# Performance work log

Hardware: AMD Instinct MI355X
Metric: run time of the kernel (lower is better)

The kernel has to match this reference:

```python
import jax, jax.numpy as jnp
import numpy as np
import math

PERIODS = [4, 2, 1]          # period_num[-3:] sorted desc
SEQ, PRED, CH = 192, 96, 8
TOPM, DM = 20, 512
N_TRAIN, BSZ = 10000, 32


def decompose_mg(data):
    # data: [N, L, C] -> mg: [P, N, L, C], offset-removed (last step per period)
    N, L, C = data.shape
    mgs = []
    for g in PERIODS:
        cur = data.reshape(N, L // g, g, C).mean(axis=2)   # pooled
        cur = jnp.repeat(cur, g, axis=1)                   # repeat_interleave
        mgs.append(cur)
    mg = jnp.stack(mgs, axis=0)                            # [P, N, L, C]
    offset = mg[:, :, -1:, :]
    return mg - offset


def l2norm(x, eps=1e-12):
    n = jnp.sqrt(jnp.sum(x * x, axis=-1, keepdims=True))
    return x / jnp.maximum(n, eps)


def setup_inputs() -> dict:
    key = jax.random.key(0)
    ks = jax.random.split(key, 10)
    F = SEQ * CH
    return {
        "x": jax.random.normal(ks[0], (BSZ, SEQ, CH), dtype=jnp.float32),
        "index": jax.random.randint(ks[1], (BSZ,), 0, N_TRAIN),
        "train_data_all": jax.random.normal(ks[2], (N_TRAIN, SEQ, CH), dtype=jnp.float32),
        "y_data_all": jax.random.normal(ks[3], (N_TRAIN, PRED, CH), dtype=jnp.float32),
        "W_sim": jax.random.normal(ks[4], (F, F), dtype=jnp.float32) / math.sqrt(F),
        "b_sim": jax.random.normal(ks[5], (F,), dtype=jnp.float32) * 0.01,
        "Wq": jax.random.normal(ks[6], (CH, DM), dtype=jnp.float32) / math.sqrt(CH),
        "bq": jax.random.normal(ks[7], (DM,), dtype=jnp.float32) * 0.01,
        "Wk": jax.random.normal(ks[8], (CH, DM), dtype=jnp.float32) / math.sqrt(CH),
        "bk": jax.random.normal(ks[9], (DM,), dtype=jnp.float32) * 0.01,
    }


def reference(x, index, train_data_all, y_data_all, W_sim, b_sim, Wq, bq, Wk, bk):
    P = len(PERIODS)
    bsz = x.shape[0]
    n_train = train_data_all.shape[0]

    # multi-period decomposition (prepare_dataset + retrieve)
    train_mg = decompose_mg(train_data_all)   # [P, N, SEQ, CH]
    y_mg = decompose_mg(y_data_all)           # [P, N, PRED, CH]
    x_mg = decompose_mg(x)                    # [P, B, SEQ, CH]

    # periodic_batch_corr: shared linear then cosine similarity
    bx = x_mg.reshape(P, bsz, -1) @ W_sim + b_sim           # [P, B, F]
    ax = train_mg.reshape(P, n_train, -1) @ W_sim + b_sim   # [P, N, F]
    sim = jnp.einsum('pbf,pnf->pbn', l2norm(bx), l2norm(ax))

    # self-exclusion sliding mask (train=True)
    win = 2 * (SEQ + PRED) - 1
    slid = jnp.arange(win)[None, :] + (index - SEQ - PRED + 1)[:, None]
    slid = jnp.clip(slid, 0, n_train - 1)
    mask = jnp.zeros((bsz, n_train), dtype=bool).at[
        jnp.arange(bsz)[:, None], slid].set(True)
    sim = jnp.where(mask[None], -jnp.inf, sim)

    # top-m retrieval
    _, topm_idx = jax.lax.top_k(sim, TOPM)                  # [P, B, TOPM]

    # gather neighbors per period
    gather = jax.vmap(lambda src, i: src[i])                # over period axis
    k = gather(train_mg, topm_idx)                          # [P, B, M, SEQ, CH]
    v = gather(y_mg, topm_idx)                              # [P, B, M, PRED, CH]

    # cross attention (shared projections across periods)
    q_emb = x_mg @ Wq + bq                                  # [P, B, S, D]
    k_emb = k @ Wk + bk                                     # [P, B, M, T, D]
    scores = jnp.einsum('pbsd,pbmtd->pbsmt', q_emb, k_emb) / math.sqrt(DM)
    S = scores.shape[2]
    w = jax.nn.softmax(scores.reshape(P, bsz, S, TOPM * S), axis=-1)
    w = w.reshape(P, bsz, S, TOPM, S)
    nw = w.sum(axis=-1).sum(axis=2)                         # [P, B, M]
    nw = jax.nn.softmax(nw, axis=-1)
    out = jnp.einsum('pbm,pbmlc->pblc', nw, v)              # [P, B, PRED, CH]
    return out
```

## Files before the change

### kernel.cpp

```cpp
#include <hip/hip_runtime.h>
#include <hip/hip_bf16.h>
#include <math.h>

#define NPER 3
#define SEQL 192
#define PREDL 96
#define CH 8
#define FD 1536
#define NT 10000
#define BS 32
#define PB 96
#define TOPM 20
#define DM 512
#define HALFW 287
#define NROWS 30000
#define NRP2 10112
#define NRB2 79
#define NCB 12
#define PCOLS 24
#define NWG2 (NRB2*NCB)
#define NJ 3840
#define K0R 384
#define K1R 768
#define K2R 1536
#define KS 16
#define KSD 8
#define NCH 4
#define CHSZ (NT/NCH)
#define NWTG 4080
#define NB_DOT (NRB2*KSD)
#define RSQRT_DM 0.04419417382415922f

typedef __attribute__((ext_vector_type(8))) short bf16x8;
typedef __attribute__((ext_vector_type(4))) float f32x4;
typedef __attribute__((address_space(3))) short lds_short_t;
typedef __attribute__((address_space(1))) const short glb_short_t;

__device__ inline float bflo(unsigned u){ return __uint_as_float(u << 16); }
__device__ inline float bfhi(unsigned u){ return __uint_as_float(u & 0xFFFF0000u); }
__device__ inline float bf2f(unsigned short u){ return __uint_as_float((unsigned)u << 16); }
__device__ inline unsigned short f2bf(float v){
  __hip_bfloat16 h = __float2bfloat16(v);
  return *reinterpret_cast<unsigned short*>(&h);
}

template<int L>
__device__ __forceinline__ void dec_body(const float* __restrict__ data,
                                         float* __restrict__ mg,
                                         __hip_bfloat16* __restrict__ m0,
                                         __hip_bfloat16* __restrict__ m1,
                                         __hip_bfloat16* __restrict__ m2,
                                         __hip_bfloat16* __restrict__ trH,
                                         __hip_bfloat16* __restrict__ trL,
                                         int N, int n, float* fpool) {
  float* row = fpool;
  float* m4  = fpool + L*CH;
  float* m2s = fpool + L*CH + (L/4)*CH;
  const float* src = data + (size_t)n*L*CH;
  for (int e = threadIdx.x; e < L*CH/4; e += 256)
    *reinterpret_cast<float4*>(&row[e*4]) = *reinterpret_cast<const float4*>(&src[e*4]);
  __syncthreads();
  for (int i = threadIdx.x; i < (L/4)*CH; i += 256) {
    int j = i >> 3, c = i & 7;
    m4[i] = (row[(4*j)*CH+c] + row[(4*j+1)*CH+c] + row[(4*j+2)*CH+c] + row[(4*j+3)*CH+c]) * 0.25f;
  }
  for (int i = threadIdx.x; i < (L/2)*CH; i += 256) {
    int j = i >> 3, c = i & 7;
    m2s[i] = (row[(2*j)*CH+c] + row[(2*j+1)*CH+c]) * 0.5f;
  }
  __syncthreads();
  if (mg) {
    size_t plane = (size_t)N*L*CH;
    size_t base  = (size_t)n*L*CH;
    for (int e = threadIdx.x; e < L*CH/4; e += 256) {
      int i = e*4;
      int l = i >> 3, c0 = i & 7;
      float v0[4], v1[4], v2[4];
      #pragma unroll
      for (int j=0;j<4;j++) {
        int c = c0 + j;
        v0[j] = m4[(l>>2)*CH+c] - m4[(L/4-1)*CH+c];
        v1[j] = m2s[(l>>1)*CH+c] - m2s[(L/2-1)*CH+c];
        v2[j] = row[i+j] - row[(L-1)*CH+c];
      }
      *reinterpret_cast<float4*>(&mg[base+i])           = make_float4(v0[0],v0[1],v0[2],v0[3]);
      *reinterpret_cast<float4*>(&mg[plane+base+i])     = make_float4(v1[0],v1[1],v1[2],v1[3]);
      *reinterpret_cast<float4*>(&mg[2*plane+base+i])   = make_float4(v2[0],v2[1],v2[2],v2[3]);
    }
  }
  if (m0) {
    unsigned short* p0 = (unsigned short*)m0 + (size_t)n*K0R;
    unsigned short* p1 = (unsigned short*)m1 + (size_t)n*K1R;
    unsigned short* p2 = (unsigned short*)m2 + (size_t)n*K2R;
    for (int e = threadIdx.x; e < K0R/4; e += 256) {
      int i = e*4, c0 = i & 7;
      ushort4 u;
      u.x = f2bf(m4[i]   - m4[(L/4-1)*CH + c0]);
      u.y = f2bf(m4[i+1] - m4[(L/4-1)*CH + c0+1]);
      u.z = f2bf(m4[i+2] - m4[(L/4-1)*CH + c0+2]);
      u.w = f2bf(m4[i+3] - m4[(L/4-1)*CH + c0+3]);
      *reinterpret_cast<ushort4*>(&p0[i]) = u;
    }
    for (int e = threadIdx.x; e < K1R/4; e += 256) {
      int i = e*4, c0 = i & 7;
      ushort4 u;
      u.x = f2bf(m2s[i]   - m2s[(L/2-1)*CH + c0]);
      u.y = f2bf(m2s[i+1] - m2s[(L/2-1)*CH + c0+1]);
      u.z = f2bf(m2s[i+2] - m2s[(L/2-1)*CH + c0+2]);
      u.w = f2bf(m2s[i+3] - m2s[(L/2-1)*CH + c0+3]);
      *reinterpret_cast<ushort4*>(&p1[i]) = u;
    }
    for (int e = threadIdx.x; e < K2R/4; e += 256) {
      int i = e*4, c0 = i & 7;
      ushort4 u;
      u.x = f2bf(row[i]   - row[(L-1)*CH + c0]);
      u.y = f2bf(row[i+1] - row[(L-1)*CH + c0+1]);
      u.z = f2bf(row[i+2] - row[(L-1)*CH + c0+2]);
      u.w = f2bf(row[i+3] - row[(L-1)*CH + c0+3]);
      *reinterpret_cast<ushort4*>(&p2[i]) = u;
    }
  }
  if (trH) {
    unsigned short* h = (unsigned short*)trH + (size_t)n*L*CH;
    unsigned short* l = (unsigned short*)trL + (size_t)n*L*CH;
    for (int e = threadIdx.x; e < L*CH/4; e += 256) {
      int i = e*4;
      ushort4 uh, ul;
      uh.x = f2bf(row[i]);   ul.x = f2bf(row[i]   - bf2f(uh.x));
      uh.y = f2bf(row[i+1]); ul.y = f2bf(row[i+1] - bf2f(uh.y));
      uh.z = f2bf(row[i+2]); ul.z = f2bf(row[i+2] - bf2f(uh.z));
      uh.w = f2bf(row[i+3]); ul.w = f2bf(row[i+3] - bf2f(uh.w));
      *reinterpret_cast<ushort4*>(&h[i]) = uh;
      *reinterpret_cast<ushort4*>(&l[i]) = ul;
    }
  }
}

__device__ __forceinline__ void wtg_body(const float* __restrict__ W,
                                         __hip_bfloat16* __restrict__ wt0,
                                         __hip_bfloat16* __restrict__ wt1,
                                         __hip_bfloat16* __restrict__ wt2,
                                         const float* __restrict__ Wq,
                                         const float* __restrict__ bq,
                                         const float* __restrict__ Wk,
                                         const float* __restrict__ bk,
                                         float* __restrict__ cst,
                                         int wb, float* fpool) {
  int bxx = wb / 48, byy = wb % 48;
  if (bxx == 84) {
    if (byy != 0) return;
    int tt = threadIdx.x;
    if (tt < 64) {
      int c = tt >> 3, e = tt & 7;
      float s = 0.f;
      for (int d=0; d<DM; d++) s += Wq[c*DM+d] * Wk[e*DM+d];
      cst[tt] = s;
    } else if (tt < 72) {
      int c = tt - 64; float s=0.f;
      for (int d=0;d<DM;d++) s += Wq[c*DM+d]*bk[d];
      cst[tt] = s;
    } else if (tt < 80) {
      int e = tt - 72; float s=0.f;
      for (int d=0;d<DM;d++) s += Wk[e*DM+d]*bq[d];
      cst[tt] = s;
    } else if (tt == 80) {
      float s=0.f;
      for (int d=0;d<DM;d++) s += bq[d]*bk[d];
      cst[80] = s;
    }
    return;
  }
  int G, kr0, Kred;
  __hip_bfloat16* Wt;
  if (bxx < 12)      { G = 4; kr0 = bxx*32;      Kred = K0R; Wt = wt0; }
  else if (bxx < 36) { G = 2; kr0 = (bxx-12)*32; Kred = K1R; Wt = wt1; }
  else               { G = 1; kr0 = (bxx-36)*32; Kred = K2R; Wt = wt2; }
  int f0 = byy*32;
  int k0 = kr0*G;
  int tid = threadIdx.x, tx = tid & 31, ty = tid >> 5;
  for (int i = ty; i < 32*G; i += 8)
    fpool[i*33 + tx] = W[(size_t)(k0+i)*FD + f0 + tx];
  __syncthreads();
  for (int fl = ty; fl < 32; fl += 8) {
    float s = 0.f;
    for (int i=0;i<G;i++) s += fpool[(((tx>>3)*G+i)*8 + (tx&7))*33 + fl];
    Wt[(size_t)(f0+fl)*Kred + kr0 + tx] = __float2bfloat16(s);
  }
}

__global__ __launch_bounds__(256) void k_front(const float* __restrict__ x,
                                               const float* __restrict__ train,
                                               float* __restrict__ x_mg,
                                               __hip_bfloat16* __restrict__ m0,
                                               __hip_bfloat16* __restrict__ m1,
                                               __hip_bfloat16* __restrict__ m2,
                                               __hip_bfloat16* __restrict__ trH,
                                               __hip_bfloat16* __restrict__ trL,
                                               const float* __restrict__ W,
                                               __hip_bfloat16* __restrict__ wt0,
                                               __hip_bfloat16* __restrict__ wt1,
                                               __hip_bfloat16* __restrict__ wt2,
                                               const float* __restrict__ Wq,
                                               const float* __restrict__ bq,
                                               const float* __restrict__ Wk,
                                               const float* __restrict__ bk,
                                               float* __restrict__ cst) {
  __shared__ float fpool[128*33];
  int bid = blockIdx.x;
  if (bid < NT) {
    dec_body<SEQL>(train, nullptr, m0, m1, m2, trH, trL, NT, bid, fpool);
  } else if (bid < NT + NWTG) {
    wtg_body(W, wt0, wt1, wt2, Wq, bq, Wk, bk, cst, bid - NT, fpool);
  } else {
    dec_body<SEQL>(x, x_mg, nullptr, nullptr, nullptr, nullptr, nullptr,
                   BS, bid - NT - NWTG, fpool);
  }
}

__global__ __launch_bounds__(256) void k_bx_part(const float* __restrict__ xmg,
                                                 const float* __restrict__ W,
                                                 float* __restrict__ bxp) {
  __shared__ float xs[PB][17];
  __shared__ float Ws[16][65];
  int f0 = blockIdx.x * 64;
  int ks = blockIdx.y;
  int kbase = ks * (FD/KS);
  int tid = threadIdx.x;
  int fl = tid & 63, gp = tid >> 6;
  float acc[24];
  #pragma unroll
  for (int j=0;j<24;j++) acc[j]=0.f;
  for (int k0 = kbase; k0 < kbase + FD/KS; k0 += 16) {
    for (int e = tid; e < PB*16; e += 256) {
      int r = e >> 4, k = e & 15;
      xs[r][k] = xmg[(size_t)r*FD + k0 + k];
    }
    for (int e = tid; e < 16*64; e += 256) {
      int k = e >> 6, f = e & 63;
      Ws[k][f] = W[(size_t)(k0+k)*FD + f0 + f];
    }
    __syncthreads();
    #pragma unroll
    for (int kk = 0; kk < 16; kk++) {
      float w = Ws[kk][fl];
      #pragma unroll
      for (int j=0;j<24;j++) acc[j] += w * xs[gp + 4*j][kk];
    }
    __syncthreads();
  }
  #pragma unroll
  for (int j=0;j<24;j++) {
    int pb = gp + 4*j;
    bxp[((size_t)ks*PB + pb)*FD + f0 + fl] = acc[j];
  }
}

__global__ __launch_bounds__(256) void k_bxnorm(const float* __restrict__ bxp,
                                                const float* __restrict__ bsim,
                                                float* __restrict__ u_out,
                                                float* __restrict__ cpb) {
  __shared__ float rowv[FD];
  __shared__ float r1[256], r2[256];
  __shared__ float invs;
  int pb = blockIdx.x, tid = threadIdx.x;
  float s2 = 0.f, sb = 0.f;
  for (int f = tid; f < FD; f += 256) {
    float s = 0.f;
    #pragma unroll
    for (int ks=0; ks<KS; ks++) s += bxp[((size_t)ks*PB + pb)*FD + f];
    s += bsim[f];
    rowv[f] = s;
    s2 += s*s; sb += s*bsim[f];
  }
  r1[tid]=s2; r2[tid]=sb; __syncthreads();
  for (int off=128; off>0; off>>=1) {
    if (tid<off) { r1[tid]+=r1[tid+off]; r2[tid]+=r2[tid+off]; }
    __syncthreads();
  }
  if (tid==0) {
    float iv = 1.f / fmaxf(sqrtf(r1[0]), 1e-12f);
    invs = iv;
    cpb[pb] = r2[0] * iv;
  }
  __syncthreads();
  float iv = invs;
  for (int f = tid; f < FD; f += 256) u_out[(size_t)pb*FD + f] = rowv[f]*iv;
}

__global__ __launch_bounds__(256) void k_t_part(const float* __restrict__ u,
                                                const float* __restrict__ W,
                                                float* __restrict__ tp) {
  __shared__ float us[PB][17];
  __shared__ float Wt[64][17];
  int k0 = blockIdx.x * 64;
  int ks = blockIdx.y;
  int fbase = ks * (FD/KS);
  int tid = threadIdx.x;
  int kl = tid & 63, gp = tid >> 6;
  float acc[24];
  #pragma unroll
  for (int j=0;j<24;j++) acc[j]=0.f;
  for (int fc = fbase; fc < fbase + FD/KS; fc += 16) {
    for (int e = tid; e < PB*16; e += 256) {
      int r = e >> 4, f = e & 15;
      us[r][f] = u[(size_t)r*FD + fc + f];
    }
    for (int e = tid; e < 64*16; e += 256) {
      int k = e >> 4, f = e & 15;
      Wt[k][f] = W[(size_t)(k0+k)*FD + fc + f];
    }
    __syncthreads();
    #pragma unroll
    for (int ff = 0; ff < 16; ff++) {
      float w = Wt[kl][ff];
      #pragma unroll
      for (int j=0;j<24;j++) acc[j] += w * us[gp + 4*j][ff];
    }
    __syncthreads();
  }
  #pragma unroll
  for (int j=0;j<24;j++) {
    int pb = gp + 4*j;
    tp[((size_t)ks*PB + pb)*FD + k0 + kl] = acc[j];
  }
}

__global__ __launch_bounds__(192) void k_tred_adj(const float* __restrict__ tp,
                                                  __hip_bfloat16* __restrict__ tadjH,
                                                  __hip_bfloat16* __restrict__ tadjL) {
  __shared__ float ts[SEQL*CH];
  __shared__ float Tc[CH];
  int pb = blockIdx.x;
  int p = pb / BS;
  int g = (p==0) ? 4 : (p==1) ? 2 : 1;
  int l = threadIdx.x;
  #pragma unroll
  for (int c=0;c<CH;c++) {
    float s = 0.f;
    #pragma unroll
    for (int ks=0; ks<KS; ks++) s += tp[((size_t)ks*PB + pb)*FD + l*CH + c];
    ts[l*CH+c] = s;
  }
  __syncthreads();
  if (l < CH) {
    float s=0.f;
    for (int j=0;j<SEQL;j++) s += ts[j*CH+l];
    Tc[l] = s;
  }
  __syncthreads();
  int j0 = (l/g)*g;
  bool last = (j0 == SEQL-g);
  float ig = 1.f/(float)g;
  unsigned short* th = (unsigned short*)tadjH;
  unsigned short* tl = (unsigned short*)tadjL;
  #pragma unroll
  for (int c=0;c<CH;c++) {
    float s = 0.f;
    for (int jj=0;jj<g;jj++) s += ts[(j0+jj)*CH+c];
    float v = s*ig - (last ? Tc[c]*ig : 0.f);
    unsigned short hv = f2bf(v);
    th[(size_t)pb*FD + l*CH+c] = hv;
    tl[(size_t)pb*FD + l*CH+c] = f2bf(v - bf2f(hv));
  }
}

__device__ __forceinline__ void norm_body(const short* __restrict__ A,
                                          const short* __restrict__ B,
                                          int K, int p, int seg,
                                          const float* __restrict__ bsim,
                                          float* __restrict__ part,
                                          short* pool) {
  short* lA = pool;
  short* lB = pool + 128*32;
  int q = NWG2 >> 3, r = NWG2 & 7;
  int xcd = seg & 7, pos = seg >> 3;
  int wgid = (xcd < r ? xcd*(q+1) : r*(q+1) + (xcd-r)*q) + pos;
  int rb = wgid / NCB, cb = wgid - rb*NCB;
  int row0 = rb*128, col0 = cb*128;
  int tid = threadIdx.x, lane = tid & 63, wid = tid >> 6;
  int wr = (wid>>1)*64, wc = (wid&1)*64;

  size_t aoff[2], boff[2];
  int ldsb[2];
  #pragma unroll
  for (int i=0;i<2;i++) {
    int lrow = (wid*2+i)*16 + (lane>>2);
    int sl = lane & 3;
    int ss = (sl - lrow - (lrow>>2)) & 3;
    aoff[i] = (size_t)(row0 + lrow)*K + 8*ss;
    boff[i] = (size_t)(col0 + lrow)*K + 8*ss;
    ldsb[i] = (wid*2+i)*16*32;
  }

  f32x4 acc[4][4];
  #pragma unroll
  for (int m=0;m<4;m++)
    #pragma unroll
    for (int n=0;n<4;n++) acc[m][n] = (f32x4){0.f,0.f,0.f,0.f};

  int kslot = lane >> 4;
  for (int k0 = 0; k0 < K; k0 += 32) {
    #pragma unroll
    for (int i=0;i<2;i++) {
      __builtin_amdgcn_global_load_lds((glb_short_t*)(A + aoff[i] + k0),
                                       (lds_short_t*)&lA[ldsb[i]], 16, 0, 0);
      __builtin_amdgcn_global_load_lds((glb_short_t*)(B + boff[i] + k0),
                                       (lds_short_t*)&lB[ldsb[i]], 16, 0, 0);
    }
    __syncthreads();
    bf16x8 af[4], bfr[4];
    #pragma unroll
    for (int m=0;m<4;m++) {
      int rr = wr + m*16 + (lane&15);
      int s = (kslot + rr + (rr>>2)) & 3;
      af[m] = *(const bf16x8*)&lA[rr*32 + s*8];
    }
    #pragma unroll
    for (int n=0;n<4;n++) {
      int rr = wc + n*16 + (lane&15);
      int s = (kslot + rr + (rr>>2)) & 3;
      bfr[n] = *(const bf16x8*)&lB[rr*32 + s*8];
    }
    #pragma unroll
    for (int m=0;m<4;m++)
      #pragma unroll
      for (int n=0;n<4;n++)
        acc[m][n] = __builtin_amdgcn_mfma_f32_16x16x32_bf16(af[m], bfr[n], acc[m][n], 0, 0, 0);
    __syncthreads();
  }

  float bv[4];
  #pragma unroll
  for (int n=0;n<4;n++) bv[n] = bsim[col0 + wc + n*16 + (lane&15)];
  int pslot = cb*2 + (wid&1);
  #pragma unroll
  for (int m=0;m<4;m++) {
    #pragma unroll
    for (int j=0;j<4;j++) {
      float s = 0.f;
      #pragma unroll
      for (int n=0;n<4;n++) { float v = acc[m][n][j] + bv[n]; s += v*v; }
      s += __shfl_xor(s, 1); s += __shfl_xor(s, 2);
      s += __shfl_xor(s, 4); s += __shfl_xor(s, 8);
      if ((lane & 15) == 0) {
        int rr = row0 + wr + m*16 + (lane>>4)*4 + j;
        part[((size_t)p*NRP2 + rr)*PCOLS + pslot] = s;
      }
    }
  }
}

__device__ __forceinline__ void dot_body(const short* __restrict__ AH,
                                         const short* __restrict__ AL,
                                         const short* __restrict__ BH,
                                         const short* __restrict__ BL,
                                         float* __restrict__ dotp,
                                         int dbid, short* pool) {
  short* lAH = pool;
  short* lAL = pool + 128*32;
  short* lBH = pool + 2*128*32;
  short* lBL = pool + 3*128*32;
  int ks = dbid & 7, cbn = dbid >> 3;
  int col0 = cbn * 128;
  int kbase = ks * (FD/KSD);
  int tid = threadIdx.x, lane = tid & 63, wid = tid >> 6;
  int wr = (wid>>1)*64, wc = (wid&1)*64;

  size_t aoff[2], boff[2];
  int ldsb[2];
  #pragma unroll
  for (int i=0;i<2;i++) {
    int lrow = (wid*2+i)*16 + (lane>>2);
    int sl = lane & 3;
    int ss = (sl - lrow - (lrow>>2)) & 3;
    aoff[i] = (size_t)lrow*FD + 8*ss;
    boff[i] = (size_t)(col0 + lrow)*FD + 8*ss;
    ldsb[i] = (wid*2+i)*16*32;
  }

  f32x4 acc[4][4];
  #pragma unroll
  for (int m=0;m<4;m++)
    #pragma unroll
    for (int n=0;n<4;n++) acc[m][n] = (f32x4){0.f,0.f,0.f,0.f};

  int kslot = lane >> 4;
  for (int k0 = kbase; k0 < kbase + FD/KSD; k0 += 32) {
    #pragma unroll
    for (int i=0;i<2;i++) {
      __builtin_amdgcn_global_load_lds((glb_short_t*)(AH + aoff[i] + k0),
                                       (lds_short_t*)&lAH[ldsb[i]], 16, 0, 0);
      __builtin_amdgcn_global_load_lds((glb_short_t*)(AL + aoff[i] + k0),
                                       (lds_short_t*)&lAL[ldsb[i]], 16, 0, 0);
      __builtin_amdgcn_global_load_lds((glb_short_t*)(BH + boff[i] + k0),
                                       (lds_short_t*)&lBH[ldsb[i]], 16, 0, 0);
      __builtin_amdgcn_global_load_lds((glb_short_t*)(BL + boff[i] + k0),
                                       (lds_short_t*)&lBL[ldsb[i]], 16, 0, 0);
    }
    __syncthreads();
    bf16x8 ah[4], al[4], bh[4], bl[4];
    #pragma unroll
    for (int m=0;m<4;m++) {
      int rr = wr + m*16 + (lane&15);
      int s = (kslot + rr + (rr>>2)) & 3;
      ah[m] = *(const bf16x8*)&lAH[rr*32 + s*8];
      al[m] = *(const bf16x8*)&lAL[rr*32 + s*8];
    }
    #pragma unroll
    for (int n=0;n<4;n++) {
      int rr = wc + n*16 + (lane&15);
      int s = (kslot + rr + (rr>>2)) & 3;
      bh[n] = *(const bf16x8*)&lBH[rr*32 + s*8];
      bl[n] = *(const bf16x8*)&lBL[rr*32 + s*8];
    }
    #pragma unroll
    for (int m=0;m<4;m++)
      #pragma unroll
      for (int n=0;n<4;n++) {
        acc[m][n] = __builtin_amdgcn_mfma_f32_16x16x32_bf16(ah[m], bh[n], acc[m][n], 0, 0, 0);
        acc[m][n] = __builtin_amdgcn_mfma_f32_16x16x32_bf16(ah[m], bl[n], acc[m][n], 0, 0, 0);
        acc[m][n] = __builtin_amdgcn_mfma_f32_16x16x32_bf16(al[m], bh[n], acc[m][n], 0, 0, 0);
      }
    __syncthreads();
  }

  #pragma unroll
  for (int m=0;m<4;m++) {
    int prow = wr + m*16 + (lane>>4)*4;
    if (prow >= PB) continue;
    #pragma unroll
    for (int n=0;n<4;n++) {
      int ncol = col0 + wc + n*16 + (lane&15);
      if (ncol >= NT) continue;
      #pragma unroll
      for (int j=0;j<4;j++) {
        dotp[((size_t)ks*PB + prow + j)*NT + ncol] = acc[m][n][j];
      }
    }
  }
}

__global__ __launch_bounds__(256) void k_gemms(
    const __hip_bfloat16* __restrict__ A0b, const __hip_bfloat16* __restrict__ A1b,
    const __hip_bfloat16* __restrict__ A2b,
    const __hip_bfloat16* __restrict__ B0b, const __hip_bfloat16* __restrict__ B1b,
    const __hip_bfloat16* __restrict__ B2b,
    const float* __restrict__ bsim, float* __restrict__ part,
    const __hip_bfloat16* __restrict__ tadjHb, const __hip_bfloat16* __restrict__ tadjLb,
    const __hip_bfloat16* __restrict__ trHb, const __hip_bfloat16* __restrict__ trLb,
    float* __restrict__ dotp) {
  __shared__ __align__(16) short pool[4*128*32];
  int bid = blockIdx.x;
  if (bid < NWG2) {
    norm_body((const short*)A2b, (const short*)B2b, K2R, 2, bid, bsim, part, pool);
  } else if (bid < 2*NWG2) {
    norm_body((const short*)A1b, (const short*)B1b, K1R, 1, bid - NWG2, bsim, part, pool);
  } else if (bid < 2*NWG2 + NB_DOT) {
    dot_body((const short*)tadjHb, (const short*)tadjLb,
             (const short*)trHb, (const short*)trLb, dotp, bid - 2*NWG2, pool);
  } else {
    norm_body((const short*)A0b, (const short*)B0b, K0R, 0,
              bid - 2*NWG2 - NB_DOT, bsim, part, pool);
  }
}

__global__ __launch_bounds__(256) void k_norm_red(const float* __restrict__ part,
                                                  float* __restrict__ norm2) {
  int r = blockIdx.x*256 + threadIdx.x;
  if (r < NROWS) {
    int p = r / NT, rr = r - p*NT;
    float s=0.f;
    #pragma unroll
    for (int cb=0; cb<PCOLS; cb++) s += part[((size_t)p*NRP2 + rr)*PCOLS + cb];
    norm2[r] = s;
  }
}

__global__ __launch_bounds__(256) void k_topk_part(const float* __restrict__ dotp,
                                                   const float* __restrict__ cpb,
                                                   const float* __restrict__ norm2,
                                                   const int* __restrict__ index,
                                                   float* __restrict__ cv,
                                                   int* __restrict__ ci) {
  __shared__ float vals[CHSZ];
  __shared__ float rv[4];
  __shared__ int   ri[4];
  int pb = blockIdx.x, ch = blockIdx.y;
  int p = pb / BS, b = pb - p*BS;
  int n0 = ch*CHSZ;
  int tid = threadIdx.x, lane = tid & 63, wv = tid >> 6;
  int idx = index[b];
  int bl = idx - HALFW; if (bl < 0) bl = 0;
  int bh = idx + HALFW; if (bh > NT-1) bh = NT-1;
  const float* n2 = norm2 + (size_t)p*NT;
  float cp = cpb[pb];
  for (int i = tid; i < CHSZ; i += 256) {
    int n = n0 + i;
    float d = 0.f;
    #pragma unroll
    for (int ks=0; ks<KSD; ks++) d += dotp[((size_t)ks*PB + pb)*NT + n];
    d += cp;
    float v = d / fmaxf(sqrtf(n2[n]), 1e-12f);
    if (n >= bl && n <= bh) v = -INFINITY;
    vals[i] = v;
  }
  __syncthreads();
  for (int it = 0; it < TOPM; it++) {
    float bv = -INFINITY; int bi = CHSZ;
    for (int i = tid; i < CHSZ; i += 256) {
      float v = vals[i];
      if (v > bv) { bv = v; bi = i; }
    }
    #pragma unroll
    for (int off=32; off>0; off>>=1) {
      float ov = __shfl_xor(bv, off);
      int   oi = __shfl_xor(bi, off);
      if (ov > bv || (ov == bv && oi < bi)) { bv = ov; bi = oi; }
    }
    if (lane == 0) { rv[wv] = bv; ri[wv] = bi; }
    __syncthreads();
    if (tid == 0) {
      float fv = rv[0]; int fi = ri[0];
      #pragma unroll
      for (int w2=1; w2<4; w2++)
        if (rv[w2] > fv || (rv[w2] == fv && ri[w2] < fi)) { fv = rv[w2]; fi = ri[w2]; }
      cv[(pb*NCH + ch)*TOPM + it] = fv;
      ci[(pb*NCH + ch)*TOPM + it] = n0 + fi;
      vals[fi] = -INFINITY;
    }
    __syncthreads();
  }
}

__global__ __launch_bounds__(64) void k_topk_merge(const float* __restrict__ cv,
                                                   const int* __restrict__ ci,
                                                   int* __restrict__ topm) {
  __shared__ float v[NCH*TOPM];
  __shared__ int   id[NCH*TOPM];
  int pb = blockIdx.x;
  int lane = threadIdx.x;
  for (int i = lane; i < NCH*TOPM; i += 64) {
    v[i]  = cv[pb*NCH*TOPM + i];
    id[i] = ci[pb*NCH*TOPM + i];
  }
  __syncthreads();
  for (int it = 0; it < TOPM; it++) {
    float bv = -INFINITY; int bi = 0x7fffffff;
    for (int i = lane; i < NCH*TOPM; i += 64) {
      float vv = v[i];
      int ii = id[i];
      if (vv > bv || (vv == bv && ii < bi)) { bv = vv; bi = ii; }
    }
    #pragma unroll
    for (int off=32; off>0; off>>=1) {
      float ov = __shfl_xor(bv, off);
      int   oi = __shfl_xor(bi, off);
      if (ov > bv || (ov == bv && oi < bi)) { bv = ov; bi = oi; }
    }
    if (lane == 0) topm[pb*TOPM + it] = bi;
    for (int i = lane; i < NCH*TOPM; i += 64)
      if (id[i] == bi) v[i] = -INFINITY;
    __syncthreads();
  }
}

__device__ __forceinline__ void v_body(const float* __restrict__ ydata,
                                       const int* __restrict__ topm,
                                       float* __restrict__ vbuf,
                                       int bm, float* bpool) {
  float* row = bpool;
  float* m4  = bpool + 768;
  float* m2  = bpool + 960;
  int pb = bm / TOPM;
  int p = pb / BS;
  int n = topm[bm];
  int tid = threadIdx.x;
  const float* src = ydata + (size_t)n*PREDL*CH;
  for (int i=tid; i<PREDL*CH; i+=256) row[i]=src[i];
  __syncthreads();
  for (int i=tid; i<(PREDL/4)*CH; i+=256) {
    int j=i>>3, c=i&7;
    m4[i] = (row[(4*j)*CH+c]+row[(4*j+1)*CH+c]+row[(4*j+2)*CH+c]+row[(4*j+3)*CH+c])*0.25f;
  }
  for (int i=tid; i<(PREDL/2)*CH; i+=256) {
    int j=i>>3, c=i&7;
    m2[i] = (row[(2*j)*CH+c]+row[(2*j+1)*CH+c])*0.5f;
  }
  __syncthreads();
  float* dst = vbuf + (size_t)bm*PREDL*CH;
  for (int i=tid; i<PREDL*CH; i+=256) {
    int l=i>>3, c=i&7;
    float v;
    if (p==0)      v = m4[(l>>2)*CH+c] - m4[(PREDL/4-1)*CH+c];
    else if (p==1) v = m2[(l>>1)*CH+c] - m2[(PREDL/2-1)*CH+c];
    else           v = row[i] - row[(PREDL-1)*CH+c];
    dst[i] = v;
  }
}

template<int SH>
__device__ __forceinline__ void scores_body(
    const short* __restrict__ plane, int Kp,
    int pb, int sg,
    const int* __restrict__ topm,
    const float* __restrict__ xmg,
    const float* __restrict__ cst,
    float* __restrict__ nws,
    float* sc, int* tl, float* wred, float* lcst) {
  constexpr int UNQ = SEQL >> SH;
  constexpr int J   = TOPM * UNQ;
  constexpr int NU  = (J + 255) >> 8;
  constexpr bool FULL = (J % 256 == 0);
  int tid = threadIdx.x;
  int lane = tid & 63, wv = tid >> 6;
  if (tid < TOPM) tl[tid] = topm[pb*TOPM + tid];
  if (tid >= 32 && tid < 32+81) lcst[tid-32] = cst[tid-32];
  __syncthreads();
  uint4 kreg[NU];
  #pragma unroll
  for (int u=0; u<NU; u++) {
    int j = tid + u*256;
    if (FULL || j < J) {
      int m = j / UNQ, jj = j - m*UNQ;
      kreg[u] = *reinterpret_cast<const uint4*>(plane + (size_t)tl[m]*Kp + jj*8);
    }
  }
  for (int s8 = 0; s8 < 8; s8++) {
    int s = sg*8 + s8;
    int qr = pb*SEQL + s;
    float4 qa = *reinterpret_cast<const float4*>(&xmg[(size_t)qr*8]);
    float4 qc = *reinterpret_cast<const float4*>(&xmg[(size_t)qr*8+4]);
    float xq[8] = {qa.x,qa.y,qa.z,qa.w,qc.x,qc.y,qc.z,qc.w};
    float q[8];
    #pragma unroll
    for (int e=0;e<8;e++) {
      float ss = lcst[72+e];
      #pragma unroll
      for (int c=0;c<8;c++) ss += xq[c]*lcst[c*8+e];
      q[e] = ss;
    }
    float qb_s = lcst[80];
    #pragma unroll
    for (int c=0;c<8;c++) qb_s += xq[c]*lcst[64+c];
    float ms[NU];
    float lmax = -INFINITY;
    #pragma unroll
    for (int u=0; u<NU; u++) {
      int j = tid + u*256;
      if (FULL || j < J) {
        uint4 w = kreg[u];
        float s0 = qb_s;
        s0 += q[0]*bflo(w.x) + q[1]*bfhi(w.x);
        s0 += q[2]*bflo(w.y) + q[3]*bfhi(w.y);
        s0 += q[4]*bflo(w.z) + q[5]*bfhi(w.z);
        s0 += q[6]*bflo(w.w) + q[7]*bfhi(w.w);
        s0 *= RSQRT_DM;
        ms[u] = s0;
        lmax = fmaxf(lmax, s0);
      } else ms[u] = -INFINITY;
    }
    #pragma unroll
    for (int off=32; off>0; off>>=1) lmax = fmaxf(lmax, __shfl_xor(lmax, off));
    if (lane==0) wred[wv] = lmax;
    __syncthreads();
    float mx = fmaxf(fmaxf(wred[0],wred[1]),fmaxf(wred[2],wred[3]));
    float lsum = 0.f;
    #pragma unroll
    for (int u=0; u<NU; u++) {
      int j = tid + u*256;
      if (FULL || j < J) {
        float e = __expf(ms[u]-mx);
        sc[j] = e;
        lsum += e;
      }
    }
    #pragma unroll
    for (int off=32; off>0; off>>=1) lsum += __shfl_xor(lsum, off);
    if (lane==0) wred[4+wv] = lsum;
    __syncthreads();
    float invZ = 1.f / (wred[4]+wred[5]+wred[6]+wred[7]);
    for (int m = wv; m < TOPM; m += 4) {
      float v = 0.f;
      #pragma unroll
      for (int jj = 0; jj < UNQ; jj += 64) {
        int j2 = jj + lane;
        if (UNQ % 64 == 0 || j2 < UNQ) v += sc[m*UNQ + j2];
      }
      #pragma unroll
      for (int off=32; off>0; off>>=1) v += __shfl_xor(v, off);
      if (lane==0) nws[((size_t)pb*SEQL + s)*TOPM + m] = v * invZ;
    }
    __syncthreads();
  }
}

__global__ __launch_bounds__(256) void k_back(const __hip_bfloat16* __restrict__ m0,
                                              const __hip_bfloat16* __restrict__ m1,
                                              const __hip_bfloat16* __restrict__ m2,
                                              const int* __restrict__ topm,
                                              const float* __restrict__ xmg,
                                              const float* __restrict__ cst,
                                              float* __restrict__ nws,
                                              const float* __restrict__ ydata,
                                              float* __restrict__ vbuf) {
  __shared__ float bpool[3968];
  int bid = blockIdx.x;
  if (bid < PB*24) {
    int pb = bid / 24, sg = bid - (bid/24)*24;
    int p = pb / BS;
    float* sc = bpool;
    int* tl = (int*)(bpool + 3840);
    float* wred = bpool + 3864;
    float* lcst = bpool + 3872;
    if (p == 0)
      scores_body<2>((const short*)m0, K0R, pb, sg, topm, xmg, cst, nws, sc, tl, wred, lcst);
    else if (p == 1)
      scores_body<1>((const short*)m1, K1R, pb, sg, topm, xmg, cst, nws, sc, tl, wred, lcst);
    else
      scores_body<0>((const short*)m2, K2R, pb, sg, topm, xmg, cst, nws, sc, tl, wred, lcst);
  } else {
    v_body(ydata, topm, vbuf, bid - PB*24, bpool);
  }
}

__global__ __launch_bounds__(256) void k_out(const float* __restrict__ nws,
                                             const float* __restrict__ vbuf,
                                             float* __restrict__ out) {
  __shared__ float nwp[TOPM];
  __shared__ float nwf[TOPM];
  int pb = blockIdx.x;
  int tid = threadIdx.x;
  if (tid < TOPM) {
    float s=0.f;
    for (int ss=0; ss<SEQL; ss++) s += nws[((size_t)pb*SEQL+ss)*TOPM + tid];
    nwp[tid] = s;
  }
  __syncthreads();
  if (tid==0) {
    float mx=-INFINITY;
    for (int m=0;m<TOPM;m++) mx=fmaxf(mx,nwp[m]);
    float Z=0.f;
    for (int m=0;m<TOPM;m++){ float e=expf(nwp[m]-mx); nwf[m]=e; Z+=e; }
    float iz=1.f/Z;
    for (int m=0;m<TOPM;m++) nwf[m]*=iz;
  }
  __syncthreads();
  for (int i=tid; i<PREDL*CH; i+=256) {
    float o=0.f;
    #pragma unroll
    for (int m=0;m<TOPM;m++) o += nwf[m]*vbuf[((size_t)pb*TOPM+m)*PREDL*CH + i];
    out[(size_t)pb*PREDL*CH + i] = o;
  }
}

extern "C" void kernel_launch(void* const* d_in, const int* in_sizes, int n_in,
                              void* d_out, int out_size, void* d_ws, size_t ws_size,
                              hipStream_t stream) {
  const float* x     = (const float*)d_in[0];
  const int*   index = (const int*)  d_in[1];
  const float* train = (const float*)d_in[2];
  const float* ydata = (const float*)d_in[3];
  const float* Wsim  = (const float*)d_in[4];
  const float* bsim  = (const float*)d_in[5];
  const float* Wq    = (const float*)d_in[6];
  const float* bq    = (const float*)d_in[7];
  const float* Wk    = (const float*)d_in[8];
  const float* bk    = (const float*)d_in[9];
  float* out = (float*)d_out;

  float* ws = (float*)d_ws;
  size_t off = 0;
  auto alloc = [&](size_t n)->float* { float* pp = ws + off; off += (n + 63) & ~(size_t)63; return pp; };
  __hip_bfloat16* m0b = (__hip_bfloat16*)alloc((size_t)NRP2*K0R/2);
  __hip_bfloat16* m1b = (__hip_bfloat16*)alloc((size_t)NRP2*K1R/2);
  __hip_bfloat16* m2b = (__hip_bfloat16*)alloc((size_t)NRP2*K2R/2);
  __hip_bfloat16* wt0 = (__hip_bfloat16*)alloc((size_t)FD*K0R/2);
  __hip_bfloat16* wt1 = (__hip_bfloat16*)alloc((size_t)FD*K1R/2);
  __hip_bfloat16* wt2 = (__hip_bfloat16*)alloc((size_t)FD*K2R/2);
  __hip_bfloat16* trH = (__hip_bfloat16*)alloc((size_t)NRP2*FD/2);
  __hip_bfloat16* trL = (__hip_bfloat16*)alloc((size_t)NRP2*FD/2);
  __hip_bfloat16* tadjH = (__hip_bfloat16*)alloc((size_t)128*FD/2);
  __hip_bfloat16* tadjL = (__hip_bfloat16*)alloc((size_t)128*FD/2);
  float* x_mg     = alloc((size_t)NPER*BS*FD);
  float* bx       = alloc((size_t)PB*FD);
  float* cpb      = alloc(PB);
  float* gpart    = alloc((size_t)KS*PB*FD);
  float* part     = alloc((size_t)NPER*NRP2*PCOLS);
  float* norm2    = alloc(NROWS);
  float* dotp     = alloc((size_t)KSD*PB*NT);
  float* cv       = alloc((size_t)PB*NCH*TOPM);
  int*   ci       = (int*)alloc(PB*NCH*TOPM);
  int*   topm     = (int*)alloc(PB*TOPM);
  float* cst      = alloc(128);
  float* vbuf     = alloc((size_t)PB*TOPM*PREDL*CH);
  float* nws      = alloc((size_t)PB*SEQL*TOPM);
  if (off * sizeof(float) > ws_size) return;

  k_front<<<NT + NWTG + BS, 256, 0, stream>>>(x, train, x_mg, m0b, m1b, m2b, trH, trL,
                                              Wsim, wt0, wt1, wt2, Wq, bq, Wk, bk, cst);
  k_bx_part<<<dim3(24, KS), 256, 0, stream>>>(x_mg, Wsim, gpart);
  k_bxnorm<<<PB, 256, 0, stream>>>(gpart, bsim, bx, cpb);
  k_t_part<<<dim3(24, KS), 256, 0, stream>>>(bx, Wsim, gpart);
  k_tred_adj<<<PB, 192, 0, stream>>>(gpart, tadjH, tadjL);
  k_gemms<<<3*NWG2 + NB_DOT, 256, 0, stream>>>(m0b, m1b, m2b, wt0, wt1, wt2, bsim, part,
                                               tadjH, tadjL, trH, trL, dotp);
  k_norm_red<<<(NROWS+255)/256, 256, 0, stream>>>(part, norm2);
  k_topk_part<<<dim3(PB, NCH), 256, 0, stream>>>(dotp, cpb, norm2, index, cv, ci);
  k_topk_merge<<<PB, 64, 0, stream>>>(cv, ci, topm);
  k_back<<<PB*24 + PB*TOPM, 256, 0, stream>>>(m0b, m1b, m2b, topm, x_mg, cst, nws,
                                              ydata, vbuf);
  k_out<<<PB, 256, 0, stream>>>(nws, vbuf, out);
}
```

Baseline: 425.0 us.

## Drop split-K in dot GEMM, load A fragments directly, schedule dot blocks first

After: 431.8 us. Within noise of the previous version (+1.6%).

```diff
diff --git a/kernel.cpp b/kernel.cpp
--- a/kernel.cpp
+++ b/kernel.cpp
@@ -24,11 +24,10 @@
 #define K1R 768
 #define K2R 1536
 #define KS 16
-#define KSD 8
 #define NCH 4
 #define CHSZ (NT/NCH)
 #define NWTG 4080
-#define NB_DOT (NRB2*KSD)
+#define NB_DOT NRB2
 #define RSQRT_DM 0.04419417382415922f
 
 typedef __attribute__((ext_vector_type(8))) short bf16x8;
@@ -454,29 +453,27 @@
                                          const short* __restrict__ AL,
                                          const short* __restrict__ BH,
                                          const short* __restrict__ BL,
-                                         float* __restrict__ dotp,
-                                         int dbid, short* pool) {
-  short* lAH = pool;
-  short* lAL = pool + 128*32;
-  short* lBH = pool + 2*128*32;
-  short* lBL = pool + 3*128*32;
-  int ks = dbid & 7, cbn = dbid >> 3;
+                                         float* __restrict__ dot,
+                                         int cbn, short* pool) {
+  short* lBH = pool;
+  short* lBL = pool + 128*32;
   int col0 = cbn * 128;
-  int kbase = ks * (FD/KSD);
   int tid = threadIdx.x, lane = tid & 63, wid = tid >> 6;
   int wr = (wid>>1)*64, wc = (wid&1)*64;
 
-  size_t aoff[2], boff[2];
+  size_t boff[2];
   int ldsb[2];
   #pragma unroll
   for (int i=0;i<2;i++) {
     int lrow = (wid*2+i)*16 + (lane>>2);
     int sl = lane & 3;
     int ss = (sl - lrow - (lrow>>2)) & 3;
-    aoff[i] = (size_t)lrow*FD + 8*ss;
     boff[i] = (size_t)(col0 + lrow)*FD + 8*ss;
     ldsb[i] = (wid*2+i)*16*32;
   }
+  size_t abase[4];
+  #pragma unroll
+  for (int m=0;m<4;m++) abase[m] = (size_t)(wr + m*16 + (lane&15))*FD + (lane>>4)*8;
 
   f32x4 acc[4][4];
   #pragma unroll
@@ -485,27 +482,22 @@
     for (int n=0;n<4;n++) acc[m][n] = (f32x4){0.f,0.f,0.f,0.f};
 
   int kslot = lane >> 4;
-  for (int k0 = kbase; k0 < kbase + FD/KSD; k0 += 32) {
+  for (int k0 = 0; k0 < FD; k0 += 32) {
     #pragma unroll
     for (int i=0;i<2;i++) {
-      __builtin_amdgcn_global_load_lds((glb_short_t*)(AH + aoff[i] + k0),
-                                       (lds_short_t*)&lAH[ldsb[i]], 16, 0, 0);
-      __builtin_amdgcn_global_load_lds((glb_short_t*)(AL + aoff[i] + k0),
-                                       (lds_short_t*)&lAL[ldsb[i]], 16, 0, 0);
       __builtin_amdgcn_global_load_lds((glb_short_t*)(BH + boff[i] + k0),
                                        (lds_short_t*)&lBH[ldsb[i]], 16, 0, 0);
       __builtin_amdgcn_global_load_lds((glb_short_t*)(BL + boff[i] + k0),
                                        (lds_short_t*)&lBL[ldsb[i]], 16, 0, 0);
     }
-    __syncthreads();
-    bf16x8 ah[4], al[4], bh[4], bl[4];
+    bf16x8 ah[4], al[4];
     #pragma unroll
     for (int m=0;m<4;m++) {
-      int rr = wr + m*16 + (lane&15);
-      int s = (kslot + rr + (rr>>2)) & 3;
-      ah[m] = *(const bf16x8*)&lAH[rr*32 + s*8];
-      al[m] = *(const bf16x8*)&lAL[rr*32 + s*8];
-    }
+      ah[m] = *(const bf16x8*)&AH[abase[m] + k0];
+      al[m] = *(const bf16x8*)&AL[abase[m] + k0];
+    }
+    __syncthreads();
+    bf16x8 bh[4], bl[4];
     #pragma unroll
     for (int n=0;n<4;n++) {
       int rr = wc + n*16 + (lane&15);
@@ -534,7 +526,7 @@
       if (ncol >= NT) continue;
       #pragma unroll
       for (int j=0;j<4;j++) {
-        dotp[((size_t)ks*PB + prow + j)*NT + ncol] = acc[m][n][j];
+        dot[(size_t)(prow + j)*NT + ncol] = acc[m][n][j];
       }
     }
   }
@@ -548,19 +540,19 @@
     const float* __restrict__ bsim, float* __restrict__ part,
     const __hip_bfloat16* __restrict__ tadjHb, const __hip_bfloat16* __restrict__ tadjLb,
     const __hip_bfloat16* __restrict__ trHb, const __hip_bfloat16* __restrict__ trLb,
-    float* __restrict__ dotp) {
-  __shared__ __align__(16) short pool[4*128*32];
+    float* __restrict__ dotb) {
+  __shared__ __align__(16) short pool[2*128*32];
   int bid = blockIdx.x;
-  if (bid < NWG2) {
-    norm_body((const short*)A2b, (const short*)B2b, K2R, 2, bid, bsim, part, pool);
-  } else if (bid < 2*NWG2) {
-    norm_body((const short*)A1b, (const short*)B1b, K1R, 1, bid - NWG2, bsim, part, pool);
-  } else if (bid < 2*NWG2 + NB_DOT) {
+  if (bid < NB_DOT) {
     dot_body((const short*)tadjHb, (const short*)tadjLb,
-             (const short*)trHb, (const short*)trLb, dotp, bid - 2*NWG2, pool);
+             (const short*)trHb, (const short*)trLb, dotb, bid, pool);
+  } else if (bid < NB_DOT + NWG2) {
+    norm_body((const short*)A2b, (const short*)B2b, K2R, 2, bid - NB_DOT, bsim, part, pool);
+  } else if (bid < NB_DOT + 2*NWG2) {
+    norm_body((const short*)A1b, (const short*)B1b, K1R, 1, bid - NB_DOT - NWG2, bsim, part, pool);
   } else {
     norm_body((const short*)A0b, (const short*)B0b, K0R, 0,
-              bid - 2*NWG2 - NB_DOT, bsim, part, pool);
+              bid - NB_DOT - 2*NWG2, bsim, part, pool);
   }
 }
 
@@ -576,7 +568,7 @@
   }
 }
 
-__global__ __launch_bounds__(256) void k_topk_part(const float* __restrict__ dotp,
+__global__ __launch_bounds__(256) void k_topk_part(const float* __restrict__ dotb,
                                                    const float* __restrict__ cpb,
                                                    const float* __restrict__ norm2,
                                                    const int* __restrict__ index,
@@ -596,10 +588,7 @@
   float cp = cpb[pb];
   for (int i = tid; i < CHSZ; i += 256) {
     int n = n0 + i;
-    float d = 0.f;
-    #pragma unroll
-    for (int ks=0; ks<KSD; ks++) d += dotp[((size_t)ks*PB + pb)*NT + n];
-    d += cp;
+    float d = dotb[(size_t)pb*NT + n] + cp;
     float v = d / fmaxf(sqrtf(n2[n]), 1e-12f);
     if (n >= bl && n <= bh) v = -INFINITY;
     vals[i] = v;
@@ -887,7 +876,7 @@
   float* gpart    = alloc((size_t)KS*PB*FD);
   float* part     = alloc((size_t)NPER*NRP2*PCOLS);
   float* norm2    = alloc(NROWS);
-  float* dotp     = alloc((size_t)KSD*PB*NT);
+  float* dotb     = alloc((size_t)PB*NT);
   float* cv       = alloc((size_t)PB*NCH*TOPM);
   int*   ci       = (int*)alloc(PB*NCH*TOPM);
   int*   topm     = (int*)alloc(PB*TOPM);
@@ -902,10 +891,10 @@
   k_bxnorm<<<PB, 256, 0, stream>>>(gpart, bsim, bx, cpb);
   k_t_part<<<dim3(24, KS), 256, 0, stream>>>(bx, Wsim, gpart);
   k_tred_adj<<<PB, 192, 0, stream>>>(gpart, tadjH, tadjL);
-  k_gemms<<<3*NWG2 + NB_DOT, 256, 0, stream>>>(m0b, m1b, m2b, wt0, wt1, wt2, bsim, part,
-                                               tadjH, tadjL, trH, trL, dotp);
+  k_gemms<<<NB_DOT + 3*NWG2, 256, 0, stream>>>(m0b, m1b, m2b, wt0, wt1, wt2, bsim, part,
+                                               tadjH, tadjL, trH, trL, dotb);
   k_norm_red<<<(NROWS+255)/256, 256, 0, stream>>>(part, norm2);
-  k_topk_part<<<dim3(PB, NCH), 256, 0, stream>>>(dotp, cpb, norm2, index, cv, ci);
+  k_topk_part<<<dim3(PB, NCH), 256, 0, stream>>>(dotb, cpb, norm2, index, cv, ci);
   k_topk_merge<<<PB, 64, 0, stream>>>(cv, ci, topm);
   k_back<<<PB*24 + PB*TOPM, 256, 0, stream>>>(m0b, m1b, m2b, topm, x_mg, cst, nws,
                                               ydata, vbuf);
```
